# Optimization experiments

Measured on AMD Instinct MI355X. Metric: run time of the kernel, lower is better.

## Reference

```python
import jax, jax.numpy as jnp
import numpy as np

N = 8192        # nodes
D_IN = 256      # in_dims
D_OUT = 32      # out_dims (assignment clusters)


def setup_inputs() -> dict:
    key = jax.random.key(0)
    k1, k2, k3 = jax.random.split(key, 3)
    main_feat = jax.random.normal(k1, (N, D_IN), dtype=jnp.float32)
    main_adj = jax.random.uniform(k2, (N, N), dtype=jnp.float32)
    W = jax.random.normal(k3, (D_IN, D_OUT), dtype=jnp.float32) * (1.0 / np.sqrt(D_IN))
    b = jnp.zeros((D_OUT,), dtype=jnp.float32)
    return {"main_feat": main_feat, "main_adj": main_adj, "W": W, "b": b}


def reference(main_feat, main_adj, W, b):
    # GraphConvolution: support = X @ W ; out = A @ support + b   -> [N, D_OUT]
    support = main_feat @ W
    assign = main_adj @ support + b
    # softmax over the NODE axis (dim 0), matching F.softmax(main_assign, 0)
    assign = jax.nn.softmax(assign, axis=0)
    # pooling: raw_emb = assign^T @ X  -> [D_OUT, D_IN]
    raw_emb = assign.T @ main_feat
    return raw_emb
```

## Files before the change

kernel.cpp:

```cpp
#include <hip/hip_runtime.h>
#include <stdint.h>

#define NN   8192
#define DIN  256
#define DOUT 32
#define NCHUNK 8
#define NP4   128

typedef short bf16x8 __attribute__((ext_vector_type(8)));
typedef float f32x16 __attribute__((ext_vector_type(16)));

union BF8 { uint32_t u[4]; bf16x8 v; };

__device__ __forceinline__ void split_pair(float a, float b, uint32_t& hp, uint32_t& lp) {
    uint32_t ua = __float_as_uint(a), ub = __float_as_uint(b);
    hp = (ua >> 16) | (ub & 0xffff0000u);
    float la = a - __uint_as_float(ua & 0xffff0000u);
    float lb = b - __uint_as_float(ub & 0xffff0000u);
    lp = (__float_as_uint(la) >> 16) | (__float_as_uint(lb) & 0xffff0000u);
}

__global__ __launch_bounds__(256) void k1_support(
    const float* __restrict__ X, const float* __restrict__ W,
    unsigned short* __restrict__ hi_frag, unsigned short* __restrict__ lo_frag)
{
    __shared__ float Xs[32 * 256];
    int t = threadIdx.x;
    int kbase = blockIdx.x * 32;

    const float4* Xg = (const float4*)(X + (size_t)kbase * DIN);
    float4* Xs4 = (float4*)Xs;
#pragma unroll
    for (int p = 0; p < 8; ++p) Xs4[p * 256 + t] = Xg[p * 256 + t];
    __syncthreads();

    int c = t & 31;
    int q = t >> 5;
    int kb2  = q >> 2;
    int half = (q >> 1) & 1;
    int j4   = q & 1;
    int krow0 = kb2 * 16 + half * 8 + j4 * 4;

    float acc[4] = {0.f, 0.f, 0.f, 0.f};
    for (int d = 0; d < 256; ++d) {
        float w = W[d * 32 + c];
#pragma unroll
        for (int jj = 0; jj < 4; ++jj)
            acc[jj] += Xs[(krow0 + jj) * 256 + d] * w;
    }

    uint32_t h01, l01, h23, l23;
    split_pair(acc[0], acc[1], h01, l01);
    split_pair(acc[2], acc[3], h23, l23);

    int ks = (kbase >> 4) + kb2;
    size_t elembase = (size_t)ks * 512 + (size_t)(half * 32 + c) * 8 + j4 * 4;
    *(uint2*)(hi_frag + elembase) = make_uint2(h01, h23);
    *(uint2*)(lo_frag + elembase) = make_uint2(l01, l23);
}

__global__ __launch_bounds__(256) void k2_logits(
    const float* __restrict__ adj,
    const unsigned short* __restrict__ hi_frag,
    const unsigned short* __restrict__ lo_frag,
    float* __restrict__ part)
{
    int t = threadIdx.x;
    int lane = t & 63, wv = t >> 6;
    int row_tile = blockIdx.x * 128 + wv * 32;
    int r  = lane & 31;
    int hs = lane >> 5;

    const float* arow = adj + (size_t)(row_tile + r) * NN + blockIdx.y * 1024 + hs * 8;
    const unsigned short* hp = hi_frag + (size_t)blockIdx.y * 64 * 512 + lane * 8;
    const unsigned short* lp = lo_frag + (size_t)blockIdx.y * 64 * 512 + lane * 8;

    f32x16 acc;
#pragma unroll
    for (int i = 0; i < 16; ++i) acc[i] = 0.f;

#pragma unroll 4
    for (int s = 0; s < 64; ++s) {
        float4 a0 = *(const float4*)arow;
        float4 a1 = *(const float4*)(arow + 4);
        BF8 bh, bl, ah, al;
        bh.v = *(const bf16x8*)hp;
        bl.v = *(const bf16x8*)lp;
        split_pair(a0.x, a0.y, ah.u[0], al.u[0]);
        split_pair(a0.z, a0.w, ah.u[1], al.u[1]);
        split_pair(a1.x, a1.y, ah.u[2], al.u[2]);
        split_pair(a1.z, a1.w, ah.u[3], al.u[3]);
        acc = __builtin_amdgcn_mfma_f32_32x32x16_bf16(ah.v, bh.v, acc, 0, 0, 0);
        acc = __builtin_amdgcn_mfma_f32_32x32x16_bf16(ah.v, bl.v, acc, 0, 0, 0);
        acc = __builtin_amdgcn_mfma_f32_32x32x16_bf16(al.v, bh.v, acc, 0, 0, 0);
        arow += 16; hp += 512; lp += 512;
    }

    float* pdst = part + (size_t)blockIdx.y * (NN * DOUT);
#pragma unroll
    for (int reg = 0; reg < 16; ++reg) {
        int rt = (reg & 3) + 8 * (reg >> 2) + 4 * hs;
        pdst[(size_t)(row_tile + rt) * 32 + r] = acc[reg];
    }
}

__global__ __launch_bounds__(256) void k3a_sum_max(
    const float* __restrict__ part, float* __restrict__ logits_sum,
    float* __restrict__ Mpart)
{
    __shared__ float red[256 * 4];
    int t = threadIdx.x;
    size_t f = (size_t)blockIdx.x * 256 + t;

    float4 v = ((const float4*)part)[f];
#pragma unroll
    for (int p = 1; p < NCHUNK; ++p) {
        float4 u = ((const float4*)(part + (size_t)p * NN * DOUT))[f];
        v.x += u.x; v.y += u.y; v.z += u.z; v.w += u.w;
    }
    ((float4*)logits_sum)[f] = v;

    red[t * 4 + 0] = v.x; red[t * 4 + 1] = v.y;
    red[t * 4 + 2] = v.z; red[t * 4 + 3] = v.w;
    __syncthreads();
    for (int s = 128; s >= 8; s >>= 1) {
        if (t < s)
#pragma unroll
            for (int j = 0; j < 4; ++j)
                red[t * 4 + j] = fmaxf(red[t * 4 + j], red[(t + s) * 4 + j]);
        __syncthreads();
    }
    if (t < 8)
#pragma unroll
        for (int j = 0; j < 4; ++j)
            Mpart[blockIdx.x * 32 + t * 4 + j] = red[t * 4 + j];
}

__global__ __launch_bounds__(256) void k3b_exp_sum(
    const float* __restrict__ logits_sum, const float* __restrict__ Mpart,
    float* __restrict__ e_buf, float* __restrict__ Spart)
{
    __shared__ float redm[8 * 32];
    __shared__ float Ms[32];
    __shared__ float red[256 * 4];
    int t = threadIdx.x;
    int c = t & 31, g = t >> 5;

    float m = -3.4e38f;
#pragma unroll
    for (int i = 0; i < 32; ++i)
        m = fmaxf(m, Mpart[(g + 8 * i) * 32 + c]);
    redm[g * 32 + c] = m;
    __syncthreads();
    for (int s = 4; s >= 1; s >>= 1) {
        if (g < s) redm[g * 32 + c] = fmaxf(redm[g * 32 + c], redm[(g + s) * 32 + c]);
        __syncthreads();
    }
    if (t < 32) Ms[t] = redm[t];
    __syncthreads();

    int cg = t & 7;
    float m0 = Ms[4 * cg], m1 = Ms[4 * cg + 1], m2 = Ms[4 * cg + 2], m3 = Ms[4 * cg + 3];
    size_t f = (size_t)blockIdx.x * 256 + t;
    float4 v = ((const float4*)logits_sum)[f];
    v.x = __expf(v.x - m0); v.y = __expf(v.y - m1);
    v.z = __expf(v.z - m2); v.w = __expf(v.w - m3);
    ((float4*)e_buf)[f] = v;

    red[t * 4 + 0] = v.x; red[t * 4 + 1] = v.y;
    red[t * 4 + 2] = v.z; red[t * 4 + 3] = v.w;
    __syncthreads();
    for (int s = 128; s >= 8; s >>= 1) {
        if (t < s)
#pragma unroll
            for (int j = 0; j < 4; ++j)
                red[t * 4 + j] += red[(t + s) * 4 + j];
        __syncthreads();
    }
    if (t < 8)
#pragma unroll
        for (int j = 0; j < 4; ++j)
            Spart[blockIdx.x * 32 + t * 4 + j] = red[t * 4 + j];
}

__global__ __launch_bounds__(256) void k4_pool(
    const float* __restrict__ X, const float* __restrict__ e_buf,
    float* __restrict__ p4)
{
    __shared__ float Xs[8 * 256];
    __shared__ float As[8 * 32];
    int t = threadIdx.x;
    int c = t & 31, dg = t >> 5;
    int ibase = blockIdx.x * 64;

    float acc[32];
#pragma unroll
    for (int i = 0; i < 32; ++i) acc[i] = 0.f;

    for (int rnd = 0; rnd < 8; ++rnd) {
        __syncthreads();
        const float4* Xg = (const float4*)(X + (size_t)(ibase + rnd * 8) * DIN);
        float4* Xs4 = (float4*)Xs;
        Xs4[t]       = Xg[t];
        Xs4[256 + t] = Xg[256 + t];
        As[t] = e_buf[(size_t)(ibase + rnd * 8 + (t >> 5)) * 32 + (t & 31)];
        __syncthreads();
#pragma unroll
        for (int i2 = 0; i2 < 8; ++i2) {
            float a = As[i2 * 32 + c];
#pragma unroll
            for (int dd = 0; dd < 32; ++dd)
                acc[dd] += a * Xs[i2 * 256 + dg * 32 + dd];
        }
    }
    float* dst = p4 + (size_t)blockIdx.x * (DOUT * DIN) + (size_t)c * 256 + dg * 32;
#pragma unroll
    for (int v = 0; v < 8; ++v)
        ((float4*)dst)[v] = make_float4(acc[v * 4], acc[v * 4 + 1], acc[v * 4 + 2], acc[v * 4 + 3]);
}

__global__ __launch_bounds__(256) void k5_reduce(
    const float* __restrict__ p4, const float* __restrict__ Spart,
    float* __restrict__ out)
{
    __shared__ float red[256];
    int t = threadIdx.x, b = blockIdx.x;

    red[t] = Spart[t * 32 + b];
    __syncthreads();
    for (int s = 128; s >= 1; s >>= 1) {
        if (t < s) red[t] += red[t + s];
        __syncthreads();
    }
    float invS = 1.0f / red[0];

    int j = b * 256 + t;
    float a = 0.f;
    for (int g = 0; g < NP4; ++g) a += p4[(size_t)g * (DOUT * DIN) + j];
    out[j] = a * invS;
}

extern "C" void kernel_launch(void* const* d_in, const int* in_sizes, int n_in,
                              void* d_out, int out_size, void* d_ws, size_t ws_size,
                              hipStream_t stream) {
    const float* X   = (const float*)d_in[0];
    const float* adj = (const float*)d_in[1];
    const float* W   = (const float*)d_in[2];
    float* out = (float*)d_out;

    char* w = (char*)d_ws;
    unsigned short* hi_frag = (unsigned short*)w;
    unsigned short* lo_frag = (unsigned short*)(w + 512 * 1024);
    float* part       = (float*)(w + 1 * 1024 * 1024);
    float* logits_sum = (float*)(w + 9 * 1024 * 1024);
    float* e_buf      = (float*)(w + 10 * 1024 * 1024);
    float* Mpart      = (float*)(w + 11 * 1024 * 1024);
    float* Spart      = (float*)(w + 11 * 1024 * 1024 + 32768);
    float* p4         = (float*)(w + 11 * 1024 * 1024 + 65536);

    k1_support<<<NN / 32, 256, 0, stream>>>(X, W, hi_frag, lo_frag);
    k2_logits<<<dim3(NN / 128, NCHUNK), 256, 0, stream>>>(adj, hi_frag, lo_frag, part);
    k3a_sum_max<<<256, 256, 0, stream>>>(part, logits_sum, Mpart);
    k3b_exp_sum<<<256, 256, 0, stream>>>(logits_sum, Mpart, e_buf, Spart);
    k4_pool<<<NP4, 256, 0, stream>>>(X, e_buf, p4);
    k5_reduce<<<DOUT, 256, 0, stream>>>(p4, Spart, out);
}
```

Baseline: 443.3 us.

## Fuse split-K reduction into logits kernel and exp/sum into pooling kernel

The last-arriving block for each row tile of the logits kernel, found with an atomic counter, now sums the split-K partials and computes per-tile column maxima, which removes the separate sum/max kernel. The exp and column-sum step moves into the pooling kernel, which reduces the global max on the fly and produces partial exp sums, so the e_buf round trip and one more launch go away. This cuts two kernel launches and some global traffic. The cost is a serialized tail in the last-arriving blocks, plus threadfence and atomic overhead.

```diff
diff --git a/kernel.cpp b/kernel.cpp
--- a/kernel.cpp
+++ b/kernel.cpp
@@ -22,11 +22,14 @@
 
 __global__ __launch_bounds__(256) void k1_support(
     const float* __restrict__ X, const float* __restrict__ W,
-    unsigned short* __restrict__ hi_frag, unsigned short* __restrict__ lo_frag)
+    unsigned short* __restrict__ hi_frag, unsigned short* __restrict__ lo_frag,
+    int* __restrict__ cnt)
 {
     __shared__ float Xs[32 * 256];
     int t = threadIdx.x;
     int kbase = blockIdx.x * 32;
+
+    if (blockIdx.x == 0 && t < 64) cnt[t] = 0;
 
     const float4* Xg = (const float4*)(X + (size_t)kbase * DIN);
     float4* Xs4 = (float4*)Xs;
@@ -63,7 +66,10 @@
     const float* __restrict__ adj,
     const unsigned short* __restrict__ hi_frag,
     const unsigned short* __restrict__ lo_frag,
-    float* __restrict__ part)
+    float* __restrict__ part,
+    float* __restrict__ logits_sum,
+    float* __restrict__ Mpart,
+    int* __restrict__ cnt)
 {
     int t = threadIdx.x;
     int lane = t & 63, wv = t >> 6;
@@ -102,26 +108,33 @@
         int rt = (reg & 3) + 8 * (reg >> 2) + 4 * hs;
         pdst[(size_t)(row_tile + rt) * 32 + r] = acc[reg];
     }
-}
-
-__global__ __launch_bounds__(256) void k3a_sum_max(
-    const float* __restrict__ part, float* __restrict__ logits_sum,
-    float* __restrict__ Mpart)
-{
+
+    __threadfence();
+    __shared__ int last;
+    if (t == 0) last = (atomicAdd(&cnt[blockIdx.x], 1) == NCHUNK - 1);
+    __syncthreads();
+    if (!last) return;
+    __threadfence();
+
     __shared__ float red[256 * 4];
-    int t = threadIdx.x;
-    size_t f = (size_t)blockIdx.x * 256 + t;
-
-    float4 v = ((const float4*)part)[f];
-#pragma unroll
-    for (int p = 1; p < NCHUNK; ++p) {
-        float4 u = ((const float4*)(part + (size_t)p * NN * DOUT))[f];
-        v.x += u.x; v.y += u.y; v.z += u.z; v.w += u.w;
-    }
-    ((float4*)logits_sum)[f] = v;
-
-    red[t * 4 + 0] = v.x; red[t * 4 + 1] = v.y;
-    red[t * 4 + 2] = v.z; red[t * 4 + 3] = v.w;
+    int cg = t & 7, rg = t >> 3;
+    float mx[4] = {-3.4e38f, -3.4e38f, -3.4e38f, -3.4e38f};
+#pragma unroll
+    for (int k = 0; k < 4; ++k) {
+        int row = blockIdx.x * 128 + rg + 32 * k;
+        size_t f = (size_t)row * 8 + cg;
+        float4 v = ((const float4*)part)[f];
+#pragma unroll
+        for (int p = 1; p < NCHUNK; ++p) {
+            float4 u = ((const float4*)(part + (size_t)p * NN * DOUT))[f];
+            v.x += u.x; v.y += u.y; v.z += u.z; v.w += u.w;
+        }
+        ((float4*)logits_sum)[f] = v;
+        mx[0] = fmaxf(mx[0], v.x); mx[1] = fmaxf(mx[1], v.y);
+        mx[2] = fmaxf(mx[2], v.z); mx[3] = fmaxf(mx[3], v.w);
+    }
+#pragma unroll
+    for (int j = 0; j < 4; ++j) red[t * 4 + j] = mx[j];
     __syncthreads();
     for (int s = 128; s >= 8; s >>= 1) {
         if (t < s)
@@ -136,66 +149,35 @@
             Mpart[blockIdx.x * 32 + t * 4 + j] = red[t * 4 + j];
 }
 
-__global__ __launch_bounds__(256) void k3b_exp_sum(
-    const float* __restrict__ logits_sum, const float* __restrict__ Mpart,
-    float* __restrict__ e_buf, float* __restrict__ Spart)
-{
+__global__ __launch_bounds__(256) void k4_pool(
+    const float* __restrict__ X, const float* __restrict__ logits_sum,
+    const float* __restrict__ Mpart, float* __restrict__ p4,
+    float* __restrict__ Spart)
+{
+    __shared__ float Xs[8 * 256];
+    __shared__ float As[8 * 32];
     __shared__ float redm[8 * 32];
     __shared__ float Ms[32];
-    __shared__ float red[256 * 4];
-    int t = threadIdx.x;
-    int c = t & 31, g = t >> 5;
-
-    float m = -3.4e38f;
-#pragma unroll
-    for (int i = 0; i < 32; ++i)
-        m = fmaxf(m, Mpart[(g + 8 * i) * 32 + c]);
-    redm[g * 32 + c] = m;
-    __syncthreads();
-    for (int s = 4; s >= 1; s >>= 1) {
-        if (g < s) redm[g * 32 + c] = fmaxf(redm[g * 32 + c], redm[(g + s) * 32 + c]);
-        __syncthreads();
-    }
-    if (t < 32) Ms[t] = redm[t];
-    __syncthreads();
-
-    int cg = t & 7;
-    float m0 = Ms[4 * cg], m1 = Ms[4 * cg + 1], m2 = Ms[4 * cg + 2], m3 = Ms[4 * cg + 3];
-    size_t f = (size_t)blockIdx.x * 256 + t;
-    float4 v = ((const float4*)logits_sum)[f];
-    v.x = __expf(v.x - m0); v.y = __expf(v.y - m1);
-    v.z = __expf(v.z - m2); v.w = __expf(v.w - m3);
-    ((float4*)e_buf)[f] = v;
-
-    red[t * 4 + 0] = v.x; red[t * 4 + 1] = v.y;
-    red[t * 4 + 2] = v.z; red[t * 4 + 3] = v.w;
-    __syncthreads();
-    for (int s = 128; s >= 8; s >>= 1) {
-        if (t < s)
-#pragma unroll
-            for (int j = 0; j < 4; ++j)
-                red[t * 4 + j] += red[(t + s) * 4 + j];
-        __syncthreads();
-    }
-    if (t < 8)
-#pragma unroll
-        for (int j = 0; j < 4; ++j)
-            Spart[blockIdx.x * 32 + t * 4 + j] = red[t * 4 + j];
-}
-
-__global__ __launch_bounds__(256) void k4_pool(
-    const float* __restrict__ X, const float* __restrict__ e_buf,
-    float* __restrict__ p4)
-{
-    __shared__ float Xs[8 * 256];
-    __shared__ float As[8 * 32];
     int t = threadIdx.x;
     int c = t & 31, dg = t >> 5;
     int ibase = blockIdx.x * 64;
 
+    float m = -3.4e38f;
+#pragma unroll
+    for (int i = 0; i < 8; ++i)
+        m = fmaxf(m, Mpart[(dg + 8 * i) * 32 + c]);
+    redm[dg * 32 + c] = m;
+    __syncthreads();
+    for (int s = 4; s >= 1; s >>= 1) {
+        if (dg < s) redm[dg * 32 + c] = fmaxf(redm[dg * 32 + c], redm[(dg + s) * 32 + c]);
+        __syncthreads();
+    }
+    if (t < 32) Ms[t] = redm[t];
+
     float acc[32];
 #pragma unroll
     for (int i = 0; i < 32; ++i) acc[i] = 0.f;
+    float se = 0.f;
 
     for (int rnd = 0; rnd < 8; ++rnd) {
         __syncthreads();
@@ -203,7 +185,9 @@
         float4* Xs4 = (float4*)Xs;
         Xs4[t]       = Xg[t];
         Xs4[256 + t] = Xg[256 + t];
-        As[t] = e_buf[(size_t)(ibase + rnd * 8 + (t >> 5)) * 32 + (t & 31)];
+        float e = __expf(logits_sum[(size_t)(ibase + rnd * 8 + dg) * 32 + c] - Ms[c]);
+        As[t] = e;
+        se += e;
         __syncthreads();
 #pragma unroll
         for (int i2 = 0; i2 < 8; ++i2) {
@@ -213,6 +197,16 @@
                 acc[dd] += a * Xs[i2 * 256 + dg * 32 + dd];
         }
     }
+
+    __syncthreads();
+    redm[dg * 32 + c] = se;
+    __syncthreads();
+    for (int s = 4; s >= 1; s >>= 1) {
+        if (dg < s) redm[dg * 32 + c] += redm[(dg + s) * 32 + c];
+        __syncthreads();
+    }
+    if (t < 32) Spart[blockIdx.x * 32 + t] = redm[t];
+
     float* dst = p4 + (size_t)blockIdx.x * (DOUT * DIN) + (size_t)c * 256 + dg * 32;
 #pragma unroll
     for (int v = 0; v < 8; ++v)
@@ -226,7 +220,7 @@
     __shared__ float red[256];
     int t = threadIdx.x, b = blockIdx.x;
 
-    red[t] = Spart[t * 32 + b];
+    red[t] = (t < NP4) ? Spart[t * 32 + b] : 0.f;
     __syncthreads();
     for (int s = 128; s >= 1; s >>= 1) {
         if (t < s) red[t] += red[t + s];
@@ -253,15 +247,14 @@
     unsigned short* lo_frag = (unsigned short*)(w + 512 * 1024);
     float* part       = (float*)(w + 1 * 1024 * 1024);
     float* logits_sum = (float*)(w + 9 * 1024 * 1024);
-    float* e_buf      = (float*)(w + 10 * 1024 * 1024);
-    float* Mpart      = (float*)(w + 11 * 1024 * 1024);
-    float* Spart      = (float*)(w + 11 * 1024 * 1024 + 32768);
-    float* p4         = (float*)(w + 11 * 1024 * 1024 + 65536);
-
-    k1_support<<<NN / 32, 256, 0, stream>>>(X, W, hi_frag, lo_frag);
-    k2_logits<<<dim3(NN / 128, NCHUNK), 256, 0, stream>>>(adj, hi_frag, lo_frag, part);
-    k3a_sum_max<<<256, 256, 0, stream>>>(part, logits_sum, Mpart);
-    k3b_exp_sum<<<256, 256, 0, stream>>>(logits_sum, Mpart, e_buf, Spart);
-    k4_pool<<<NP4, 256, 0, stream>>>(X, e_buf, p4);
+    float* Mpart      = (float*)(w + 10 * 1024 * 1024);
+    float* Spart      = (float*)(w + 10 * 1024 * 1024 + 8192);
+    float* p4         = (float*)(w + 10 * 1024 * 1024 + 65536);
+    int*   cnt        = (int*)  (w + 15 * 1024 * 1024);
+
+    k1_support<<<NN / 32, 256, 0, stream>>>(X, W, hi_frag, lo_frag, cnt);
+    k2_logits<<<dim3(NN / 128, NCHUNK), 256, 0, stream>>>(
+        adj, hi_frag, lo_frag, part, logits_sum, Mpart, cnt);
+    k4_pool<<<NP4, 256, 0, stream>>>(X, logits_sum, Mpart, p4, Spart);
     k5_reduce<<<DOUT, 256, 0, stream>>>(p4, Spart, out);
 }
```

Result: slower. 547.7 us (+23.6%).

## Stage adjacency tiles through LDS with direct global-to-LDS loads in logits kernel

Applied to the files above, without the earlier changes.

The logits GEMM kernel now loads each 128x64 adjacency tile into padded shared memory using global_load_lds, with rows grouped and padded to avoid bank conflicts. The MFMA operands are then read from LDS. Before, each lane did strided 32-byte reads straight from global memory. The aim is more coalesced global reads of the large adjacency matrix. The cost is two block barriers per k-step and no double buffering, so loads and compute are not overlapped.

```diff
diff --git a/kernel.cpp b/kernel.cpp
--- a/kernel.cpp
+++ b/kernel.cpp
@@ -6,6 +6,8 @@
 #define DOUT 32
 #define NCHUNK 8
 #define NP4   128
+#define GRPB 1040
+#define NGRP 32
 
 typedef short bf16x8 __attribute__((ext_vector_type(8)));
 typedef float f32x16 __attribute__((ext_vector_type(16)));
@@ -65,42 +67,66 @@
     const unsigned short* __restrict__ lo_frag,
     float* __restrict__ part)
 {
+    __shared__ char Ab[NGRP * GRPB];
     int t = threadIdx.x;
     int lane = t & 63, wv = t >> 6;
-    int row_tile = blockIdx.x * 128 + wv * 32;
-    int r  = lane & 31;
-    int hs = lane >> 5;
-
-    const float* arow = adj + (size_t)(row_tile + r) * NN + blockIdx.y * 1024 + hs * 8;
-    const unsigned short* hp = hi_frag + (size_t)blockIdx.y * 64 * 512 + lane * 8;
-    const unsigned short* lp = lo_frag + (size_t)blockIdx.y * 64 * 512 + lane * 8;
+    int strip = blockIdx.x;
+    int chunk = blockIdx.y;
+
+    int srow = lane >> 4;
+    int scol = (lane & 15) * 4;
+    const float* gbase = adj + (size_t)(strip * 128 + srow) * NN + chunk * 1024 + scol;
+
+    int r31 = lane & 31;
+    int hs  = lane >> 5;
+    int rr  = wv * 32 + r31;
+    const char* abase = Ab + (rr >> 2) * GRPB + (rr & 3) * 256 + hs * 32;
+
+    const unsigned short* hp0 = hi_frag + (size_t)chunk * 64 * 512 + lane * 8;
+    const unsigned short* lp0 = lo_frag + (size_t)chunk * 64 * 512 + lane * 8;
 
     f32x16 acc;
 #pragma unroll
     for (int i = 0; i < 16; ++i) acc[i] = 0.f;
 
-#pragma unroll 4
-    for (int s = 0; s < 64; ++s) {
-        float4 a0 = *(const float4*)arow;
-        float4 a1 = *(const float4*)(arow + 4);
-        BF8 bh, bl, ah, al;
-        bh.v = *(const bf16x8*)hp;
-        bl.v = *(const bf16x8*)lp;
-        split_pair(a0.x, a0.y, ah.u[0], al.u[0]);
-        split_pair(a0.z, a0.w, ah.u[1], al.u[1]);
-        split_pair(a1.x, a1.y, ah.u[2], al.u[2]);
-        split_pair(a1.z, a1.w, ah.u[3], al.u[3]);
-        acc = __builtin_amdgcn_mfma_f32_32x32x16_bf16(ah.v, bh.v, acc, 0, 0, 0);
-        acc = __builtin_amdgcn_mfma_f32_32x32x16_bf16(ah.v, bl.v, acc, 0, 0, 0);
-        acc = __builtin_amdgcn_mfma_f32_32x32x16_bf16(al.v, bh.v, acc, 0, 0, 0);
-        arow += 16; hp += 512; lp += 512;
-    }
-
-    float* pdst = part + (size_t)blockIdx.y * (NN * DOUT);
+    for (int kt = 0; kt < 16; ++kt) {
+#pragma unroll
+        for (int i = 0; i < 8; ++i) {
+            int g = wv * 8 + i;
+            const float* gp = gbase + (size_t)(g * 4) * NN + kt * 64;
+            __builtin_amdgcn_global_load_lds(
+                (const __attribute__((address_space(1))) void*)gp,
+                (__attribute__((address_space(3))) void*)(Ab + g * GRPB),
+                16, 0, 0);
+        }
+        bf16x8 bh[4], bl[4];
+#pragma unroll
+        for (int s = 0; s < 4; ++s) {
+            bh[s] = *(const bf16x8*)(hp0 + (size_t)(kt * 4 + s) * 512);
+            bl[s] = *(const bf16x8*)(lp0 + (size_t)(kt * 4 + s) * 512);
+        }
+        __syncthreads();
+#pragma unroll
+        for (int s = 0; s < 4; ++s) {
+            float4 a0 = *(const float4*)(abase + s * 64);
+            float4 a1 = *(const float4*)(abase + s * 64 + 16);
+            BF8 ah, al;
+            split_pair(a0.x, a0.y, ah.u[0], al.u[0]);
+            split_pair(a0.z, a0.w, ah.u[1], al.u[1]);
+            split_pair(a1.x, a1.y, ah.u[2], al.u[2]);
+            split_pair(a1.z, a1.w, ah.u[3], al.u[3]);
+            acc = __builtin_amdgcn_mfma_f32_32x32x16_bf16(ah.v, bh[s], acc, 0, 0, 0);
+            acc = __builtin_amdgcn_mfma_f32_32x32x16_bf16(ah.v, bl[s], acc, 0, 0, 0);
+            acc = __builtin_amdgcn_mfma_f32_32x32x16_bf16(al.v, bh[s], acc, 0, 0, 0);
+        }
+        __syncthreads();
+    }
+
+    float* pdst = part + (size_t)chunk * (NN * DOUT);
 #pragma unroll
     for (int reg = 0; reg < 16; ++reg) {
         int rt = (reg & 3) + 8 * (reg >> 2) + 4 * hs;
-        pdst[(size_t)(row_tile + rt) * 32 + r] = acc[reg];
+        pdst[(size_t)(strip * 128 + wv * 32 + rt) * 32 + r31] = acc[reg];
     }
 }
 
```

Result: slower. 462.8 us (+4.4%).
